# Performance work log

Measured on AMD Instinct MI355X. Metric: run time of the kernel, lower is better.

Reference implementation:

```python
import jax, jax.numpy as jnp
import numpy as np

NUM_CLASSES = 14
ATTN_DIM = 64
BN_EPS = 1e-5

def setup_inputs() -> dict:
    key = jax.random.key(0)
    ks = jax.random.split(key, 6)
    B, F = 16384, 2048
    C, D = NUM_CLASSES, ATTN_DIM
    std = 0.02
    return {
        "features": jax.random.normal(ks[0], (B, F), jnp.float32),
        "W_proj": jax.random.normal(ks[1], (F, F), jnp.float32) * std,
        "b_proj": jnp.zeros((F,), jnp.float32),
        "bn_gamma": jnp.ones((F,), jnp.float32),
        "bn_beta": jnp.zeros((F,), jnp.float32),
        "W_qk": jax.random.normal(ks[2], (C * 2 * D, F), jnp.float32) * std,
        "gamma": jax.random.normal(ks[3], (C,), jnp.float32) * 0.1,
        "W_fc": jax.random.normal(ks[4], (C, F), jnp.float32) * std,
        "b_fc": jnp.zeros((C,), jnp.float32),
    }

def reference(features, W_proj, b_proj, bn_gamma, bn_beta, W_qk, gamma, W_fc, b_fc):
    B = features.shape[0]
    C, D = NUM_CLASSES, ATTN_DIM
    # fc logits
    logits = features @ W_fc.T + b_fc  # [B, C]
    # projection: Linear -> BatchNorm1d (training-mode batch stats) -> ReLU
    h = features @ W_proj.T + b_proj  # [B, P]
    mu = jnp.mean(h, axis=0)
    var = jnp.var(h, axis=0)  # biased, as torch BN uses for normalization
    h = (h - mu) * jax.lax.rsqrt(var + BN_EPS) * bn_gamma + bn_beta
    h = jax.nn.relu(h)
    # per-class q, k
    qk = h @ W_qk.T  # [B, 2*C*D]
    q, k = jnp.split(qk, 2, axis=-1)
    q = q.reshape(B, C, D)
    k = k.reshape(B, C, D)
    attn = jnp.einsum("bcd,bed->bce", q, k)  # [B, C, C]
    diag = jnp.diagonal(attn, axis1=-2, axis2=-1)  # [B, C]
    attn = attn - diag[..., None]
    attn = attn / jnp.max(jnp.abs(attn), axis=-1, keepdims=True)
    corr = jnp.einsum("bce,be->bc", attn, jax.nn.sigmoid(logits))  # [B, C]
    return logits + gamma * corr
```

## Files before the change

### kernel.cpp

```cpp
#include <hip/hip_runtime.h>
#include <stdint.h>

#define BROWS 16384
#define FDIM  2048
#define NCLS  14
#define ADIM  64
#define NCAT  2176
#define QKN   1792

typedef __attribute__((ext_vector_type(8))) short bhalf8_t;
typedef __attribute__((ext_vector_type(4))) float f32x4_t;

__device__ __forceinline__ unsigned short f2bf(float f) {
  unsigned int u = __builtin_bit_cast(unsigned int, f);
  u += 0x7fffu + ((u >> 16) & 1u);
  return (unsigned short)(u >> 16);
}
__device__ __forceinline__ float bf2f(unsigned short s) {
  return __builtin_bit_cast(float, (unsigned int)s << 16);
}

__device__ __forceinline__ void gl_lds16(const void* g, void* l) {
  __builtin_amdgcn_global_load_lds(
      (const __attribute__((address_space(1))) unsigned int*)g,
      (__attribute__((address_space(3))) unsigned int*)l, 16, 0, 0);
}

#define BAR() do { \
    asm volatile("" ::: "memory"); \
    __builtin_amdgcn_s_barrier(); \
    asm volatile("" ::: "memory"); \
  } while (0)


__global__ void cast8_bf16(const float* __restrict__ src,
                           unsigned short* __restrict__ dst, int n8) {
  int t = blockIdx.x * 256 + threadIdx.x;
  if (t >= n8) return;
  const float4* s = (const float4*)src + 2 * (size_t)t;
  float4 a = s[0], b = s[1];
  bhalf8_t o;
  o[0] = f2bf(a.x); o[1] = f2bf(a.y); o[2] = f2bf(a.z); o[3] = f2bf(a.w);
  o[4] = f2bf(b.x); o[5] = f2bf(b.y); o[6] = f2bf(b.z); o[7] = f2bf(b.w);
  *((bhalf8_t*)dst + t) = o;
}

__global__ void build_wcat(const float* __restrict__ Wp, const float* __restrict__ Wf,
                           unsigned short* __restrict__ dst) {
  int row = blockIdx.x;
  int c8 = threadIdx.x * 8;
  const float* src = nullptr;
  if (row < 2048) src = Wp + (size_t)row * FDIM + c8;
  else if (row < 2048 + NCLS) src = Wf + (size_t)(row - 2048) * FDIM + c8;
  bhalf8_t o = {0,0,0,0,0,0,0,0};
  if (src) {
    float4 a = *(const float4*)src, b = *(const float4*)(src + 4);
    o[0] = f2bf(a.x); o[1] = f2bf(a.y); o[2] = f2bf(a.z); o[3] = f2bf(a.w);
    o[4] = f2bf(b.x); o[5] = f2bf(b.y); o[6] = f2bf(b.z); o[7] = f2bf(b.w);
  }
  *(bhalf8_t*)(dst + (size_t)row * FDIM + c8) = o;
}


template<int MODE>
__global__ __launch_bounds__(512, 2) void gemm256_bt(
    const unsigned short* __restrict__ A, const unsigned short* __restrict__ Bw,
    const float* __restrict__ bp, const float* __restrict__ bfc,
    unsigned short* __restrict__ Cb, float* __restrict__ logits,
    float* __restrict__ colsum, float* __restrict__ colsq,
    int K, int lda, int ldb, int ldc, int nBr)
{
  __shared__ unsigned short L[2][2][2][8192];

  const int t = threadIdx.x;
  const int lane = t & 63;
  const int wv = t >> 6;
  const int m = lane & 15, quad = lane >> 4;
  const int wm = wv >> 2, wn = wv & 3;

  const int nwg = gridDim.x;
  const int wg = ((blockIdx.x & 7) * (nwg >> 3)) + (blockIdx.x >> 3);
  const int bx = wg & 63;
  const int by = wg >> 6;
  const int rowBase = bx << 8;
  const int colBase = by << 8;

  const int bO = (wn & 1) << 12;
  const int ofs0 = m * 64 + ((quad ^ (m & 7)) << 3);
  const int ofs1 = ofs0 ^ 32;

  const int r0 = t >> 3;
  const int q8 = ((t ^ r0) & 7) << 3;
  const int ldD = t << 3;
  const unsigned int aOff =
      (unsigned int)(rowBase + r0) * (unsigned int)lda + (unsigned int)q8;
  unsigned int bOff00, bOff01, bOff10, bOff11;
  {
    int rr;
    rr = colBase + r0;        if (rr > nBr - 1) rr = nBr - 1;
    bOff00 = (unsigned int)rr * (unsigned int)ldb + q8;
    rr = colBase + 64 + r0;   if (rr > nBr - 1) rr = nBr - 1;
    bOff01 = (unsigned int)rr * (unsigned int)ldb + q8;
    rr = colBase + 128 + r0;  if (rr > nBr - 1) rr = nBr - 1;
    bOff10 = (unsigned int)rr * (unsigned int)ldb + q8;
    rr = colBase + 192 + r0;  if (rr > nBr - 1) rr = nBr - 1;
    bOff11 = (unsigned int)rr * (unsigned int)ldb + q8;
  }

#define STAGEA0(b, kb) do { \
    gl_lds16(A + aOff + (unsigned int)(kb), &L[b][0][0][ldD]); \
    gl_lds16(A + aOff + (unsigned int)(64 * lda) + (unsigned int)(kb), &L[b][0][0][ldD + 4096]); \
  } while (0)
#define STAGEA1(b, kb) do { \
    gl_lds16(A + aOff + (unsigned int)(128 * lda) + (unsigned int)(kb), &L[b][0][1][ldD]); \
    gl_lds16(A + aOff + (unsigned int)(192 * lda) + (unsigned int)(kb), &L[b][0][1][ldD + 4096]); \
  } while (0)
#define STAGEB0(b, kb) do { \
    gl_lds16(Bw + bOff00 + (unsigned int)(kb), &L[b][1][0][ldD]); \
    gl_lds16(Bw + bOff01 + (unsigned int)(kb), &L[b][1][0][ldD + 4096]); \
  } while (0)
#define STAGEB1(b, kb) do { \
    gl_lds16(Bw + bOff10 + (unsigned int)(kb), &L[b][1][1][ldD]); \
    gl_lds16(Bw + bOff11 + (unsigned int)(kb), &L[b][1][1][ldD + 4096]); \
  } while (0)

#define RDA(v, roff) \
    v##_0 = *(const bhalf8_t*)&LA[(roff) + ofs0]; \
    v##_1 = *(const bhalf8_t*)&LA[(roff) + ofs1];
#define RDB(v, roff) \
    v##_0 = *(const bhalf8_t*)&LB[(roff) + ofs0]; \
    v##_1 = *(const bhalf8_t*)&LB[(roff) + ofs1];
#define MM(i, j, av, bv) \
    acc[i][j] = __builtin_amdgcn_mfma_f32_16x16x32_bf16(av##_0, bv##_0, acc[i][j], 0, 0, 0); \
    acc[i][j] = __builtin_amdgcn_mfma_f32_16x16x32_bf16(av##_1, bv##_1, acc[i][j], 0, 0, 0);

  f32x4_t acc[8][4];
#pragma unroll
  for (int i = 0; i < 8; ++i)
#pragma unroll
    for (int j = 0; j < 4; ++j) acc[i][j] = (f32x4_t){0.f, 0.f, 0.f, 0.f};

  const int NT = K >> 6;

  STAGEA0(0, 0);
  STAGEA1(0, 0);
  STAGEB0(0, 0);
  STAGEB1(0, 0);
  {
    const int kb1 = (NT > 1) ? 64 : 0;
    STAGEB0(1, kb1);
    STAGEB1(1, kb1);
  }
  asm volatile("s_waitcnt vmcnt(4)" ::: "memory");
  BAR();

  for (int u = 0; u < NT; ++u) {
    const int buf = u & 1;
    const unsigned short* LA = &L[buf][0][wm][0];
    const unsigned short* LB = &L[buf][1][wn >> 1][bO];
    const int kbA = (u + 1 < NT) ? (u + 1) << 6 : 0;
    const int kbB = (u + 2 < NT) ? (u + 2) << 6 : 0;

    bhalf8_t a0_0, a0_1, a1_0, a1_1, a2_0, a2_1, a3_0, a3_1;
    bhalf8_t b0_0, b0_1, b1_0, b1_1, b2_0, b2_1, b3_0, b3_1;

    RDA(a0, 0);     RDA(a1, 1024);  RDA(a2, 2048);  RDA(a3, 3072);
    RDB(b0, 0);     RDB(b1, 1024);
    if (buf) { STAGEA0(0, kbA); } else { STAGEA0(1, kbA); }
    BAR();
    __builtin_amdgcn_s_setprio(1);
    MM(0, 0, a0, b0); MM(0, 1, a0, b1);
    MM(1, 0, a1, b0); MM(1, 1, a1, b1);
    MM(2, 0, a2, b0); MM(2, 1, a2, b1);
    MM(3, 0, a3, b0); MM(3, 1, a3, b1);
    __builtin_amdgcn_s_setprio(0);
    BAR();

    RDB(b2, 2048);  RDB(b3, 3072);
    if (buf) { STAGEA1(0, kbA); } else { STAGEA1(1, kbA); }
    BAR();
    __builtin_amdgcn_s_setprio(1);
    MM(0, 2, a0, b2); MM(0, 3, a0, b3);
    MM(1, 2, a1, b2); MM(1, 3, a1, b3);
    MM(2, 2, a2, b2); MM(2, 3, a2, b3);
    MM(3, 2, a3, b2); MM(3, 3, a3, b3);
    __builtin_amdgcn_s_setprio(0);
    BAR();

    RDA(a0, 4096);  RDA(a1, 5120);  RDA(a2, 6144);  RDA(a3, 7168);
    if (buf) { STAGEB0(1, kbB); } else { STAGEB0(0, kbB); }
    BAR();
    __builtin_amdgcn_s_setprio(1);
    MM(4, 0, a0, b0); MM(4, 1, a0, b1);
    MM(5, 0, a1, b0); MM(5, 1, a1, b1);
    MM(6, 0, a2, b0); MM(6, 1, a2, b1);
    MM(7, 0, a3, b0); MM(7, 1, a3, b1);
    __builtin_amdgcn_s_setprio(0);
    BAR();

    if (buf) { STAGEB1(1, kbB); } else { STAGEB1(0, kbB); }
    BAR();
    __builtin_amdgcn_s_setprio(1);
    MM(4, 2, a0, b2); MM(4, 3, a0, b3);
    MM(5, 2, a1, b2); MM(5, 3, a1, b3);
    MM(6, 2, a2, b2); MM(6, 3, a2, b3);
    MM(7, 2, a3, b2); MM(7, 3, a3, b3);
    __builtin_amdgcn_s_setprio(0);
    asm volatile("s_waitcnt vmcnt(4)" ::: "memory");
    BAR();
  }
  asm volatile("s_waitcnt vmcnt(0)" ::: "memory");

#undef STAGEA0
#undef STAGEA1
#undef STAGEB0
#undef STAGEB1
#undef RDA
#undef RDB
#undef MM

  if (MODE == 0) {
    if (colBase < 2048) {
#pragma unroll
      for (int ni = 0; ni < 4; ++ni) {
        const int gcol = colBase + wn * 64 + ni * 16 + m;
        const float bv = bp[gcol];
        float s = 0.f, qq = 0.f;
#pragma unroll
        for (int mi = 0; mi < 8; ++mi) {
          const size_t grow = (size_t)(rowBase + wm * 128 + mi * 16 + quad * 4);
#pragma unroll
          for (int r = 0; r < 4; ++r) {
            float v = acc[mi][ni][r] + bv;
            Cb[(grow + r) * (size_t)ldc + gcol] = f2bf(v);
            s += v; qq += v * v;
          }
        }
        s += __shfl_xor(s, 16, 64); s += __shfl_xor(s, 32, 64);
        qq += __shfl_xor(qq, 16, 64); qq += __shfl_xor(qq, 32, 64);
        if (quad == 0) { atomicAdd(&colsum[gcol], s); atomicAdd(&colsq[gcol], qq); }
      }
    } else if (wn == 0) {
      const float bv = (m < NCLS) ? bfc[m] : 0.f;
#pragma unroll
      for (int mi = 0; mi < 8; ++mi) {
        const size_t grow = (size_t)(rowBase + wm * 128 + mi * 16 + quad * 4);
#pragma unroll
        for (int r = 0; r < 4; ++r)
          logits[(grow + r) * 16 + m] = acc[mi][0][r] + bv;
      }
    }
  } else {
#pragma unroll
    for (int ni = 0; ni < 4; ++ni) {
      const int gcol = colBase + wn * 64 + ni * 16 + m;
#pragma unroll
      for (int mi = 0; mi < 8; ++mi) {
        const size_t grow = (size_t)(rowBase + wm * 128 + mi * 16 + quad * 4);
#pragma unroll
        for (int r = 0; r < 4; ++r)
          Cb[(grow + r) * (size_t)ldc + gcol] = f2bf(acc[mi][ni][r]);
      }
    }
  }
}


__global__ void bn_finalize(const float* __restrict__ cs, const float* __restrict__ cq,
                            const float* __restrict__ g, const float* __restrict__ bt,
                            float* __restrict__ scale, float* __restrict__ shift) {
  int c = blockIdx.x * 256 + threadIdx.x;
  if (c >= FDIM) return;
  const float inv = 1.f / (float)BROWS;
  float mu = cs[c] * inv;
  float var = cq[c] * inv - mu * mu;
  float sc = g[c] * rsqrtf(var + 1e-5f);
  scale[c] = sc;
  shift[c] = bt[c] - mu * sc;
}

__global__ void bn_apply(unsigned short* __restrict__ hb, const float* __restrict__ sc,
                         const float* __restrict__ sh) {
  int t = blockIdx.x * 256 + threadIdx.x;
  int row = t >> 8;
  int c8 = (t & 255) << 3;
  unsigned short* p = hb + (size_t)row * FDIM + c8;
  bhalf8_t v = *(bhalf8_t*)p;
  float4 s0 = *(const float4*)(sc + c8), s1 = *(const float4*)(sc + c8 + 4);
  float4 h0 = *(const float4*)(sh + c8), h1 = *(const float4*)(sh + c8 + 4);
  bhalf8_t o;
  o[0] = f2bf(fmaxf(bf2f((unsigned short)v[0]) * s0.x + h0.x, 0.f));
  o[1] = f2bf(fmaxf(bf2f((unsigned short)v[1]) * s0.y + h0.y, 0.f));
  o[2] = f2bf(fmaxf(bf2f((unsigned short)v[2]) * s0.z + h0.z, 0.f));
  o[3] = f2bf(fmaxf(bf2f((unsigned short)v[3]) * s0.w + h0.w, 0.f));
  o[4] = f2bf(fmaxf(bf2f((unsigned short)v[4]) * s1.x + h1.x, 0.f));
  o[5] = f2bf(fmaxf(bf2f((unsigned short)v[5]) * s1.y + h1.y, 0.f));
  o[6] = f2bf(fmaxf(bf2f((unsigned short)v[6]) * s1.z + h1.z, 0.f));
  o[7] = f2bf(fmaxf(bf2f((unsigned short)v[7]) * s1.w + h1.w, 0.f));
  *(bhalf8_t*)p = o;
}

__global__ __launch_bounds__(256) void attn_ep(
    const unsigned short* __restrict__ qk, const float* __restrict__ logits,
    const float* __restrict__ gamma, float* __restrict__ out)
{
  const int lane = threadIdx.x & 63;
  const int wv = threadIdx.x >> 6;
  const int b = blockIdx.x * 4 + wv;
  const int m = lane & 15, quad = lane >> 4;
  const unsigned short* qrow = qk + (size_t)b * QKN;
  f32x4_t acc = (f32x4_t){0.f, 0.f, 0.f, 0.f};
#pragma unroll
  for (int ks = 0; ks < 2; ++ks) {
    bhalf8_t af = {0,0,0,0,0,0,0,0}, bf = {0,0,0,0,0,0,0,0};
    if (m < NCLS) {
      af = *(const bhalf8_t*)(qrow + m * 64 + ks * 32 + quad * 8);
      bf = *(const bhalf8_t*)(qrow + 896 + m * 64 + ks * 32 + quad * 8);
    }
    acc = __builtin_amdgcn_mfma_f32_16x16x32_bf16(af, bf, acc, 0, 0, 0);
  }
  float logit_e = (m < NCLS) ? logits[(size_t)b * 16 + m] : 0.f;
  float sig = 1.f / (1.f + __expf(-logit_e));
  float corr[4];
#pragma unroll
  for (int r = 0; r < 4; ++r) {
    int c = quad * 4 + r;
    float diag = __shfl(acc[r], (lane & 48) + c, 64);
    float a = acc[r] - diag;
    float av = (m < NCLS) ? fabsf(a) : 0.f;
    av = fmaxf(av, __shfl_xor(av, 1, 64));
    av = fmaxf(av, __shfl_xor(av, 2, 64));
    av = fmaxf(av, __shfl_xor(av, 4, 64));
    av = fmaxf(av, __shfl_xor(av, 8, 64));
    float v = (m < NCLS) ? (a / av) * sig : 0.f;
    v += __shfl_xor(v, 1, 64);
    v += __shfl_xor(v, 2, 64);
    v += __shfl_xor(v, 4, 64);
    v += __shfl_xor(v, 8, 64);
    corr[r] = v;
  }
  if (m == 0) {
#pragma unroll
    for (int r = 0; r < 4; ++r) {
      int c = quad * 4 + r;
      if (c < NCLS) {
        float lc = logits[(size_t)b * 16 + c];
        out[(size_t)b * NCLS + c] = lc + gamma[c] * corr[r];
      }
    }
  }
}


extern "C" void kernel_launch(void* const* d_in, const int* in_sizes, int n_in,
                              void* d_out, int out_size, void* d_ws, size_t ws_size,
                              hipStream_t stream) {
  const float* features = (const float*)d_in[0];
  const float* W_proj   = (const float*)d_in[1];
  const float* b_proj   = (const float*)d_in[2];
  const float* bn_gamma = (const float*)d_in[3];
  const float* bn_beta  = (const float*)d_in[4];
  const float* W_qk     = (const float*)d_in[5];
  const float* gamma    = (const float*)d_in[6];
  const float* W_fc     = (const float*)d_in[7];
  const float* b_fc     = (const float*)d_in[8];
  float* out = (float*)d_out;

  char* ws = (char*)d_ws;
  unsigned short* featC   = (unsigned short*)ws;
  unsigned short* hbuf    = (unsigned short*)(ws + 67108864);
  unsigned short* WcatC   = (unsigned short*)(ws + 134217728);
  unsigned short* WqkC    = (unsigned short*)(ws + 143130624);
  unsigned short* qkC     = (unsigned short*)(ws + 150470656);
  float*          logitsB = (float*)(ws + 209190912);
  float*          colsum  = (float*)(ws + 210239488);
  float*          colsq   = (float*)(ws + 210247680);
  float*          scalev  = (float*)(ws + 210255872);
  float*          shiftv  = (float*)(ws + 210264064);

  hipMemsetAsync(colsum, 0, 16384, stream);

  cast8_bf16<<<16384, 256, 0, stream>>>(features, featC, (BROWS * FDIM) / 8);
  build_wcat<<<NCAT, 256, 0, stream>>>(W_proj, W_fc, WcatC);
  cast8_bf16<<<1792, 256, 0, stream>>>(W_qk, WqkC, (QKN * FDIM) / 8);

  gemm256_bt<0><<<576, 512, 0, stream>>>(
      featC, WcatC, b_proj, b_fc, hbuf, logitsB, colsum, colsq,
      FDIM, FDIM, FDIM, FDIM, NCAT);

  bn_finalize<<<8, 256, 0, stream>>>(colsum, colsq, bn_gamma, bn_beta, scalev, shiftv);
  bn_apply<<<16384, 256, 0, stream>>>(hbuf, scalev, shiftv);

  gemm256_bt<1><<<448, 512, 0, stream>>>(
      hbuf, WqkC, nullptr, nullptr, qkC, nullptr, nullptr, nullptr,
      FDIM, FDIM, FDIM, QKN, QKN);

  attn_ep<<<BROWS / 4, 256, 0, stream>>>(qkC, logitsB, gamma, out);
}
```

Measured before the change: 573.9 us.

## Split fc logits out of projection GEMM and merge cast and BN kernels

Moves the 14-class fc logits out of the big projection GEMM, whose extra 256-wide column tile was mostly padding, into a separate small kernel that holds W_fc in LDS. That kernel also zeroes the BN accumulators, which removes the memset. The three cast kernels are merged into one launch, and bn_finalize is folded into bn_apply, which now recomputes scale and shift per thread. An extra lgkmcnt wait is also added in the GEMM loop. The intent is to drop wasted GEMM tiles and launch overhead, at the cost of a CUDA-core fc kernel and redundant per-thread BN stat math.

New measurement: 581.5 us. No clear change (+1.3%).

```diff
diff --git a/kernel.cpp b/kernel.cpp
--- a/kernel.cpp
+++ b/kernel.cpp
@@ -5,7 +5,6 @@
 #define FDIM  2048
 #define NCLS  14
 #define ADIM  64
-#define NCAT  2176
 #define QKN   1792
 
 typedef __attribute__((ext_vector_type(8))) short bhalf8_t;
@@ -32,43 +31,103 @@
     asm volatile("" ::: "memory"); \
   } while (0)
 
-
-__global__ void cast8_bf16(const float* __restrict__ src,
-                           unsigned short* __restrict__ dst, int n8) {
+#define CN1 4194304
+#define CN2 524288
+#define CN3 458752
+#define CN4 3584
+
+__global__ void cast_all(const float* __restrict__ f, const float* __restrict__ wp,
+                         const float* __restrict__ wqk, const float* __restrict__ wf,
+                         unsigned short* __restrict__ dst) {
   int t = blockIdx.x * 256 + threadIdx.x;
-  if (t >= n8) return;
-  const float4* s = (const float4*)src + 2 * (size_t)t;
-  float4 a = s[0], b = s[1];
+  const float* src;
+  if (t < CN1) src = f + (size_t)t * 8;
+  else if (t < CN1 + CN2) src = wp + ((size_t)t - CN1) * 8;
+  else if (t < CN1 + CN2 + CN3) src = wqk + ((size_t)t - CN1 - CN2) * 8;
+  else src = wf + ((size_t)t - CN1 - CN2 - CN3) * 8;
+  float4 a = ((const float4*)src)[0], b = ((const float4*)src)[1];
   bhalf8_t o;
   o[0] = f2bf(a.x); o[1] = f2bf(a.y); o[2] = f2bf(a.z); o[3] = f2bf(a.w);
   o[4] = f2bf(b.x); o[5] = f2bf(b.y); o[6] = f2bf(b.z); o[7] = f2bf(b.w);
   *((bhalf8_t*)dst + t) = o;
 }
 
-__global__ void build_wcat(const float* __restrict__ Wp, const float* __restrict__ Wf,
-                           unsigned short* __restrict__ dst) {
-  int row = blockIdx.x;
-  int c8 = threadIdx.x * 8;
-  const float* src = nullptr;
-  if (row < 2048) src = Wp + (size_t)row * FDIM + c8;
-  else if (row < 2048 + NCLS) src = Wf + (size_t)(row - 2048) * FDIM + c8;
-  bhalf8_t o = {0,0,0,0,0,0,0,0};
-  if (src) {
-    float4 a = *(const float4*)src, b = *(const float4*)(src + 4);
-    o[0] = f2bf(a.x); o[1] = f2bf(a.y); o[2] = f2bf(a.z); o[3] = f2bf(a.w);
-    o[4] = f2bf(b.x); o[5] = f2bf(b.y); o[6] = f2bf(b.z); o[7] = f2bf(b.w);
-  }
-  *(bhalf8_t*)(dst + (size_t)row * FDIM + c8) = o;
+__global__ __launch_bounds__(256) void fc_logits(
+    const unsigned short* __restrict__ featC, const unsigned short* __restrict__ WfC,
+    const float* __restrict__ bfc, float* __restrict__ logits, float* __restrict__ colzero)
+{
+  __shared__ unsigned short lWf[NCLS * FDIM];
+  if (blockIdx.x < 4)
+    ((float4*)colzero)[blockIdx.x * 256 + (int)threadIdx.x] = (float4){0.f, 0.f, 0.f, 0.f};
+  {
+    const bhalf8_t* s = (const bhalf8_t*)WfC;
+    bhalf8_t* d = (bhalf8_t*)lWf;
+#pragma unroll
+    for (int k = 0; k < 14; ++k)
+      d[k * 256 + (int)threadIdx.x] = s[k * 256 + (int)threadIdx.x];
+  }
+  __syncthreads();
+
+  const int lane = threadIdx.x & 63, wv = threadIdx.x >> 6;
+  const int rbase = blockIdx.x * 16 + wv * 4;
+  float acc[4][NCLS];
+#pragma unroll
+  for (int i = 0; i < 4; ++i)
+#pragma unroll
+    for (int c = 0; c < NCLS; ++c) acc[i][c] = 0.f;
+
+#pragma unroll
+  for (int w = 0; w < 4; ++w) {
+    const int c8 = (w * 64 + lane) * 8;
+    float fv[4][8];
+#pragma unroll
+    for (int i = 0; i < 4; ++i) {
+      bhalf8_t fr = *(const bhalf8_t*)(featC + (size_t)(rbase + i) * FDIM + c8);
+#pragma unroll
+      for (int j = 0; j < 8; ++j) fv[i][j] = bf2f((unsigned short)fr[j]);
+    }
+#pragma unroll
+    for (int c = 0; c < NCLS; ++c) {
+      bhalf8_t wr = *(const bhalf8_t*)&lWf[c * FDIM + c8];
+      float wv8[8];
+#pragma unroll
+      for (int j = 0; j < 8; ++j) wv8[j] = bf2f((unsigned short)wr[j]);
+#pragma unroll
+      for (int i = 0; i < 4; ++i) {
+        float s = acc[i][c];
+#pragma unroll
+        for (int j = 0; j < 8; ++j) s += fv[i][j] * wv8[j];
+        acc[i][c] = s;
+      }
+    }
+  }
+#pragma unroll
+  for (int i = 0; i < 4; ++i)
+#pragma unroll
+    for (int c = 0; c < NCLS; ++c) {
+      float v = acc[i][c];
+      v += __shfl_xor(v, 1, 64);  v += __shfl_xor(v, 2, 64);
+      v += __shfl_xor(v, 4, 64);  v += __shfl_xor(v, 8, 64);
+      v += __shfl_xor(v, 16, 64); v += __shfl_xor(v, 32, 64);
+      acc[i][c] = v;
+    }
+  if (lane == 0) {
+#pragma unroll
+    for (int i = 0; i < 4; ++i)
+#pragma unroll
+      for (int c = 0; c < NCLS; ++c)
+        logits[(size_t)(rbase + i) * 16 + c] = acc[i][c] + bfc[c];
+  }
 }
 
 
 template<int MODE>
 __global__ __launch_bounds__(512, 2) void gemm256_bt(
     const unsigned short* __restrict__ A, const unsigned short* __restrict__ Bw,
-    const float* __restrict__ bp, const float* __restrict__ bfc,
-    unsigned short* __restrict__ Cb, float* __restrict__ logits,
+    const float* __restrict__ bp,
+    unsigned short* __restrict__ Cb,
     float* __restrict__ colsum, float* __restrict__ colsq,
-    int K, int lda, int ldb, int ldc, int nBr)
+    int K, int lda, int ldb, int ldc)
 {
   __shared__ unsigned short L[2][2][2][8192];
 
@@ -94,18 +153,10 @@
   const int ldD = t << 3;
   const unsigned int aOff =
       (unsigned int)(rowBase + r0) * (unsigned int)lda + (unsigned int)q8;
-  unsigned int bOff00, bOff01, bOff10, bOff11;
-  {
-    int rr;
-    rr = colBase + r0;        if (rr > nBr - 1) rr = nBr - 1;
-    bOff00 = (unsigned int)rr * (unsigned int)ldb + q8;
-    rr = colBase + 64 + r0;   if (rr > nBr - 1) rr = nBr - 1;
-    bOff01 = (unsigned int)rr * (unsigned int)ldb + q8;
-    rr = colBase + 128 + r0;  if (rr > nBr - 1) rr = nBr - 1;
-    bOff10 = (unsigned int)rr * (unsigned int)ldb + q8;
-    rr = colBase + 192 + r0;  if (rr > nBr - 1) rr = nBr - 1;
-    bOff11 = (unsigned int)rr * (unsigned int)ldb + q8;
-  }
+  const unsigned int bOff00 = (unsigned int)(colBase + r0) * (unsigned int)ldb + q8;
+  const unsigned int bOff01 = (unsigned int)(colBase + 64 + r0) * (unsigned int)ldb + q8;
+  const unsigned int bOff10 = (unsigned int)(colBase + 128 + r0) * (unsigned int)ldb + q8;
+  const unsigned int bOff11 = (unsigned int)(colBase + 192 + r0) * (unsigned int)ldb + q8;
 
 #define STAGEA0(b, kb) do { \
     gl_lds16(A + aOff + (unsigned int)(kb), &L[b][0][0][ldD]); \
@@ -167,6 +218,7 @@
     RDA(a0, 0);     RDA(a1, 1024);  RDA(a2, 2048);  RDA(a3, 3072);
     RDB(b0, 0);     RDB(b1, 1024);
     if (buf) { STAGEA0(0, kbA); } else { STAGEA0(1, kbA); }
+    asm volatile("s_waitcnt lgkmcnt(8)" ::: "memory");
     BAR();
     __builtin_amdgcn_s_setprio(1);
     MM(0, 0, a0, b0); MM(0, 1, a0, b1);
@@ -220,35 +272,24 @@
 #undef MM
 
   if (MODE == 0) {
-    if (colBase < 2048) {
-#pragma unroll
-      for (int ni = 0; ni < 4; ++ni) {
-        const int gcol = colBase + wn * 64 + ni * 16 + m;
-        const float bv = bp[gcol];
-        float s = 0.f, qq = 0.f;
-#pragma unroll
-        for (int mi = 0; mi < 8; ++mi) {
-          const size_t grow = (size_t)(rowBase + wm * 128 + mi * 16 + quad * 4);
-#pragma unroll
-          for (int r = 0; r < 4; ++r) {
-            float v = acc[mi][ni][r] + bv;
-            Cb[(grow + r) * (size_t)ldc + gcol] = f2bf(v);
-            s += v; qq += v * v;
-          }
-        }
-        s += __shfl_xor(s, 16, 64); s += __shfl_xor(s, 32, 64);
-        qq += __shfl_xor(qq, 16, 64); qq += __shfl_xor(qq, 32, 64);
-        if (quad == 0) { atomicAdd(&colsum[gcol], s); atomicAdd(&colsq[gcol], qq); }
-      }
-    } else if (wn == 0) {
-      const float bv = (m < NCLS) ? bfc[m] : 0.f;
+#pragma unroll
+    for (int ni = 0; ni < 4; ++ni) {
+      const int gcol = colBase + wn * 64 + ni * 16 + m;
+      const float bv = bp[gcol];
+      float s = 0.f, qq = 0.f;
 #pragma unroll
       for (int mi = 0; mi < 8; ++mi) {
         const size_t grow = (size_t)(rowBase + wm * 128 + mi * 16 + quad * 4);
 #pragma unroll
-        for (int r = 0; r < 4; ++r)
-          logits[(grow + r) * 16 + m] = acc[mi][0][r] + bv;
+        for (int r = 0; r < 4; ++r) {
+          float v = acc[mi][ni][r] + bv;
+          Cb[(grow + r) * (size_t)ldc + gcol] = f2bf(v);
+          s += v; qq += v * v;
+        }
       }
+      s += __shfl_xor(s, 16, 64); s += __shfl_xor(s, 32, 64);
+      qq += __shfl_xor(qq, 16, 64); qq += __shfl_xor(qq, 32, 64);
+      if (quad == 0) { atomicAdd(&colsum[gcol], s); atomicAdd(&colsq[gcol], qq); }
     }
   } else {
 #pragma unroll
@@ -265,38 +306,28 @@
   }
 }
 
-
-__global__ void bn_finalize(const float* __restrict__ cs, const float* __restrict__ cq,
-                            const float* __restrict__ g, const float* __restrict__ bt,
-                            float* __restrict__ scale, float* __restrict__ shift) {
-  int c = blockIdx.x * 256 + threadIdx.x;
-  if (c >= FDIM) return;
-  const float inv = 1.f / (float)BROWS;
-  float mu = cs[c] * inv;
-  float var = cq[c] * inv - mu * mu;
-  float sc = g[c] * rsqrtf(var + 1e-5f);
-  scale[c] = sc;
-  shift[c] = bt[c] - mu * sc;
-}
-
-__global__ void bn_apply(unsigned short* __restrict__ hb, const float* __restrict__ sc,
-                         const float* __restrict__ sh) {
+__global__ void bn_apply(unsigned short* __restrict__ hb,
+                         const float* __restrict__ cs, const float* __restrict__ cq,
+                         const float* __restrict__ g, const float* __restrict__ bt) {
   int t = blockIdx.x * 256 + threadIdx.x;
   int row = t >> 8;
   int c8 = (t & 255) << 3;
+  const float inv = 1.f / (float)BROWS;
+  float scv[8], shv[8];
+#pragma unroll
+  for (int j = 0; j < 8; ++j) {
+    float mu = cs[c8 + j] * inv;
+    float va = cq[c8 + j] * inv - mu * mu;
+    float s = g[c8 + j] * rsqrtf(va + 1e-5f);
+    scv[j] = s;
+    shv[j] = bt[c8 + j] - mu * s;
+  }
   unsigned short* p = hb + (size_t)row * FDIM + c8;
   bhalf8_t v = *(bhalf8_t*)p;
-  float4 s0 = *(const float4*)(sc + c8), s1 = *(const float4*)(sc + c8 + 4);
-  float4 h0 = *(const float4*)(sh + c8), h1 = *(const float4*)(sh + c8 + 4);
   bhalf8_t o;
-  o[0] = f2bf(fmaxf(bf2f((unsigned short)v[0]) * s0.x + h0.x, 0.f));
-  o[1] = f2bf(fmaxf(bf2f((unsigned short)v[1]) * s0.y + h0.y, 0.f));
-  o[2] = f2bf(fmaxf(bf2f((unsigned short)v[2]) * s0.z + h0.z, 0.f));
-  o[3] = f2bf(fmaxf(bf2f((unsigned short)v[3]) * s0.w + h0.w, 0.f));
-  o[4] = f2bf(fmaxf(bf2f((unsigned short)v[4]) * s1.x + h1.x, 0.f));
-  o[5] = f2bf(fmaxf(bf2f((unsigned short)v[5]) * s1.y + h1.y, 0.f));
-  o[6] = f2bf(fmaxf(bf2f((unsigned short)v[6]) * s1.z + h1.z, 0.f));
-  o[7] = f2bf(fmaxf(bf2f((unsigned short)v[7]) * s1.w + h1.w, 0.f));
+#pragma unroll
+  for (int j = 0; j < 8; ++j)
+    o[j] = f2bf(fmaxf(bf2f((unsigned short)v[j]) * scv[j] + shv[j], 0.f));
   *(bhalf8_t*)p = o;
 }
 
@@ -368,32 +399,26 @@
 
   char* ws = (char*)d_ws;
   unsigned short* featC   = (unsigned short*)ws;
-  unsigned short* hbuf    = (unsigned short*)(ws + 67108864);
-  unsigned short* WcatC   = (unsigned short*)(ws + 134217728);
-  unsigned short* WqkC    = (unsigned short*)(ws + 143130624);
-  unsigned short* qkC     = (unsigned short*)(ws + 150470656);
-  float*          logitsB = (float*)(ws + 209190912);
-  float*          colsum  = (float*)(ws + 210239488);
-  float*          colsq   = (float*)(ws + 210247680);
-  float*          scalev  = (float*)(ws + 210255872);
-  float*          shiftv  = (float*)(ws + 210264064);
-
-  hipMemsetAsync(colsum, 0, 16384, stream);
-
-  cast8_bf16<<<16384, 256, 0, stream>>>(features, featC, (BROWS * FDIM) / 8);
-  build_wcat<<<NCAT, 256, 0, stream>>>(W_proj, W_fc, WcatC);
-  cast8_bf16<<<1792, 256, 0, stream>>>(W_qk, WqkC, (QKN * FDIM) / 8);
-
-  gemm256_bt<0><<<576, 512, 0, stream>>>(
-      featC, WcatC, b_proj, b_fc, hbuf, logitsB, colsum, colsq,
-      FDIM, FDIM, FDIM, FDIM, NCAT);
-
-  bn_finalize<<<8, 256, 0, stream>>>(colsum, colsq, bn_gamma, bn_beta, scalev, shiftv);
-  bn_apply<<<16384, 256, 0, stream>>>(hbuf, scalev, shiftv);
+  unsigned short* WpC     = (unsigned short*)(ws + 67108864);
+  unsigned short* WqkC    = (unsigned short*)(ws + 75497472);
+  unsigned short* WfC     = (unsigned short*)(ws + 82837504);
+  unsigned short* hbuf    = (unsigned short*)(ws + 82894848);
+  unsigned short* qkC     = (unsigned short*)(ws + 150003712);
+  float*          logitsB = (float*)(ws + 208723968);
+  float*          colsum  = (float*)(ws + 209772544);
+  float*          colsq   = (float*)(ws + 209780736);
+
+  cast_all<<<20238, 256, 0, stream>>>(features, W_proj, W_qk, W_fc, featC);
+
+  fc_logits<<<1024, 256, 0, stream>>>(featC, WfC, b_fc, logitsB, colsum);
+
+  gemm256_bt<0><<<512, 512, 0, stream>>>(
+      featC, WpC, b_proj, hbuf, colsum, colsq, FDIM, FDIM, FDIM, FDIM);
+
+  bn_apply<<<16384, 256, 0, stream>>>(hbuf, colsum, colsq, bn_gamma, bn_beta);
 
   gemm256_bt<1><<<448, 512, 0, stream>>>(
-      hbuf, WqkC, nullptr, nullptr, qkC, nullptr, nullptr, nullptr,
-      FDIM, FDIM, FDIM, QKN, QKN);
+      hbuf, WqkC, nullptr, qkC, nullptr, nullptr, FDIM, FDIM, FDIM, QKN);
 
   attn_ep<<<BROWS / 4, 256, 0, stream>>>(qkC, logitsB, gamma, out);
 }
```
